# Kernel tuning notes

Hardware: AMD Instinct MI355X
Metric: run time of the kernel (lower is better)

Reference implementation:

```python
import jax
import jax.numpy as jnp
import numpy as np

N_WIRES = 4          # hardcoded by QLayer encoder (rx on wires 0..3)
H = N_WIRES          # hidden_dim must equal n_qubits for the gating elementwise math
T, B, D, TAGS = 512, 2048, 8, 16  # original unbinds dim 0, so dim0 = time, dim1 = batch


def apply_rx(state, theta, wire):
    """Apply RX(theta) on `wire`. state: (B,2,2,2,2) complex64, theta: (B,)."""
    st = jnp.moveaxis(state, 1 + wire, -1)
    a, b = st[..., 0], st[..., 1]
    th = theta[:, None, None, None] * 0.5
    c = jnp.cos(th)
    s = -1j * jnp.sin(th)
    st = jnp.stack([c * a + s * b, s * a + c * b], axis=-1)
    return jnp.moveaxis(st, -1, 1 + wire)


def apply_cnot(state, ctrl, tgt):
    st = jnp.moveaxis(state, (1 + ctrl, 1 + tgt), (-2, -1))  # (...,2,2)
    st = st.at[..., 1, :].set(st[..., 1, ::-1])
    return jnp.moveaxis(st, (-2, -1), (1 + ctrl, 1 + tgt))


def qlayer(angles, thetas):
    """QuantumQLSTM.QLayer: RX data encoding, trainable RX, CNOT ring, PauliZ expvals.
    angles: (B, 4) data angles; thetas: (4,) trainable RX angles -> (B, 4) expvals."""
    bsz = angles.shape[0]
    state = jnp.zeros((bsz, 16), jnp.complex64).at[:, 0].set(1.0)
    state = state.reshape(bsz, 2, 2, 2, 2)
    for w in range(N_WIRES):
        state = apply_rx(state, angles[:, w], w)
    for w in range(N_WIRES):
        state = apply_rx(state, jnp.broadcast_to(thetas[w], (bsz,)), w)
    for w in range(N_WIRES):  # cnot(w, w+1), last wraps to 0
        state = apply_cnot(state, w, (w + 1) % N_WIRES)
    probs = state.real ** 2 + state.imag ** 2  # (B,2,2,2,2)
    exps = []
    for w in range(N_WIRES):
        sign = jnp.array([1.0, -1.0], jnp.float32).reshape(
            [1] + [2 if i == w else 1 for i in range(N_WIRES)])
        exps.append(jnp.sum(probs * sign, axis=(1, 2, 3, 4)))
    return jnp.stack(exps, axis=-1)  # (B, 4)


def lstm_forward(x, w_gates, b_gates, rx_theta):
    # Faithful to torch: inputs.unbind(dim=0) -> scan over axis 0; batch = x.shape[1].
    bsz = x.shape[1]
    h0 = jnp.zeros((bsz, H), x.dtype)
    c0 = jnp.zeros((bsz, H), x.dtype)

    def step(carry, xt):
        hx, cx = carry
        comb = jnp.concatenate([xt, hx], axis=-1)                    # (B, D+H)
        pre = jnp.einsum('bd,gkd->gbk', comb, w_gates) + b_gates[:, None, :]  # (4,B,4)
        f = jax.nn.sigmoid(qlayer(pre[0], rx_theta[0]))
        i = jax.nn.sigmoid(qlayer(pre[1], rx_theta[1]))
        g = jnp.tanh(qlayer(pre[2], rx_theta[2]))
        o = jax.nn.sigmoid(qlayer(pre[3], rx_theta[3]))
        cx = f * cx + i * g
        hx = o * jnp.tanh(cx)
        return (hx, cx), hx

    _, outs = jax.lax.scan(jax.checkpoint(step), (h0, c0), x)
    return outs  # (T, B, H)


def setup_inputs() -> dict:
    key = jax.random.key(0)
    ks = jax.random.split(key, 6)
    x = jax.random.normal(ks[0], (T, B, D), jnp.float32)
    w_gates = jax.random.normal(ks[1], (4, N_WIRES, D + H), jnp.float32) * 0.3
    b_gates = jnp.zeros((4, N_WIRES), jnp.float32)
    rx_theta = jax.random.uniform(ks[2], (4, N_WIRES), jnp.float32, 0.0, 2.0 * np.pi)
    w_tag = jax.random.normal(ks[3], (TAGS, H), jnp.float32) * 0.3
    b_tag = jnp.zeros((TAGS,), jnp.float32)
    return {"x": x, "w_gates": w_gates, "b_gates": b_gates,
            "rx_theta": rx_theta, "w_tag": w_tag, "b_tag": b_tag}


def reference(x, w_gates, b_gates, rx_theta, w_tag, b_tag):
    # encode(): SamplerQNN has input_params=[], so it cannot transform features;
    # features pass through to the QLSTM (see notes).
    outs = lstm_forward(x, w_gates, b_gates, rx_theta)   # (T, B, H)
    logits = outs @ w_tag.T + b_tag                      # (T, B, TAGS)
    return jax.nn.log_softmax(logits, axis=-1)
```

## Files before the change

kernel.cpp:

```cpp
#include <hip/hip_runtime.h>

#define TT   512
#define BB   2048
#define NTAG 16
#define CH   8
#define NCH  (TT / CH)
#define BBN  (BB * NTAG)

typedef float v2f __attribute__((ext_vector_type(2)));

#define DPP_XOR1  0xB1
#define DPP_XOR2  0x4E
#define DPP_XOR3  0x1B
#define DPP_ROR4  0x124
#define DPP_ROR8  0x128
#define DPP_ROR12 0x12C

template<int CTRL>
__device__ __forceinline__ float dppf(float v) {
    int r = __builtin_amdgcn_update_dpp(0, __builtin_bit_cast(int, v),
                                        CTRL, 0xF, 0xF, true);
    return __builtin_bit_cast(float, r);
}

__global__ __launch_bounds__(256, 1) void qlstm_fused(
    const float* __restrict__ x,
    const float* __restrict__ w_gates,
    const float* __restrict__ b_gates,
    const float* __restrict__ rx_theta,
    const float* __restrict__ w_tag,
    const float* __restrict__ b_tag,
    float* __restrict__ out)
{
    __shared__ float4 lds4[2][2][CH][8];
    __shared__ float  hbuf[2][2][CH][64];

    const int tid = threadIdx.x;
    const int wv  = tid >> 6;
    const int l   = tid & 63;
    const int e   = l >> 4;
    const int g   = (l >> 2) & 3;
    const int k   = l & 3;

    const float IV  = 0.15915494309189535f;
    const float L2E = 1.44269504088896f;
    const float LN2 = 0.69314718056f;

    if (wv < 2) {
        const int b0 = blockIdx.x * 8 + wv * 4;

        const float* wrow = w_gates + (g * 4 + k) * 12;
        const v2f wp0 = { wrow[0] * IV, wrow[1] * IV };
        const v2f wp1 = { wrow[2] * IV, wrow[3] * IV };
        const v2f wp2 = { wrow[4] * IV, wrow[5] * IV };
        const v2f wp3 = { wrow[6] * IV, wrow[7] * IV };
        const float wh0 = wrow[8 + (k ^ 0)] * IV;
        const float wh1 = wrow[8 + (k ^ 1)] * IV;
        const float wh2 = wrow[8 + (k ^ 2)] * IV;
        const float wh3 = wrow[8 + (k ^ 3)] * IV;
        const v2f bp = { (b_gates[g * 4 + k] + rx_theta[g * 4 + k]) * IV, 0.0f };

        const bool gt = (g == 2);
        const float bA = gt ? 0.0f : 0.5f;
        const float d0 = gt ? 0.999904f  : 0.25f;
        const float d1 = gt ? -0.331065f : -0.0208333333f;
        const float d2 = gt ? 0.120472f  : 0.00208333333f;
        const float d3 = gt ? -0.027717f : -2.10813e-4f;

        const float u0 = 0.999160f,  u1 = -0.325289f, u2 = 0.112257f;
        const float u3 = -0.028766f, u4 = 0.0043665f, u5 = -0.00028186f;

        const bool k0 = (k == 0), k1 = (k == 1), k3 = (k == 3);
        const bool g0 = (g == 0), g2 = (g == 2), glo = (g < 2);

        const float* xlane = x + (size_t)(l >> 3) * (BB * 8)
                               + (size_t)b0 * 8 + (l & 7) * 4;
        const size_t CHOFF = (size_t)CH * BB * 8;
        float4* ldsw = (float4*)&lds4[wv][0][0][0];

        float4 reg = *(const float4*)(xlane);
        ldsw[l] = reg;
        reg = *(const float4*)(xlane + CHOFF);

        float4 xcA = lds4[wv][0][0][2 * e];
        float4 xcB = lds4[wv][0][0][2 * e + 1];

        float h = 0.f, c = 0.f, h1 = 0.f, h2 = 0.f, h3 = 0.f;

        for (int cc = 0; cc < NCH; ++cc) {
            const int cur = cc & 1;
            ldsw[(cur ^ 1) * 64 + l] = reg;
            const int cn = (cc + 2 < NCH) ? cc + 2 : NCH - 1;
            reg = *(const float4*)(xlane + (size_t)cn * CHOFF);

            #pragma unroll
            for (int i = 0; i < CH; ++i) {
                const int nb = (i == CH - 1) ? (cur ^ 1) : cur;
                const int ns = (i + 1) & (CH - 1);
                const float4 xnA = lds4[wv][nb][ns][2 * e];
                const float4 xnB = lds4[wv][nb][ns][2 * e + 1];

                const v2f a01 = { xcA.x, xcA.y }, a23 = { xcA.z, xcA.w };
                const v2f a45 = { xcB.x, xcB.y }, a67 = { xcB.z, xcB.w };
                v2f acc = __builtin_elementwise_fma(a01, wp0, bp);
                acc = __builtin_elementwise_fma(a23, wp1, acc);
                acc = __builtin_elementwise_fma(a45, wp2, acc);
                acc = __builtin_elementwise_fma(a67, wp3, acc);
                const float accx = acc.x + acc.y;

                float ang = fmaf(h,  wh0, accx);
                ang = fmaf(h1, wh1, ang);
                ang = fmaf(h2, wh2, ang);
                ang = fmaf(h3, wh3, ang);

                const float C = __builtin_amdgcn_cosf(ang);
                const float m1 = dppf<DPP_XOR1>(C);
                const float m2 = dppf<DPP_XOR2>(C);
                const float m3 = dppf<DPP_XOR3>(C);
                const float Bp = m2 * m3;
                const float pp = C * m1;
                const float X  = k0 ? m1 : (k3 ? pp : C);
                const float Y  = k1 ? m1 : Bp;
                const float q  = X * Y;

                const float y  = q * q;
                const float y2 = y * y;
                const float tA = fmaf(y, d1, d0);
                const float tB = fmaf(y, d3, d2);
                const float P  = fmaf(y2, tB, tA);
                const float act = fmaf(q, P, bA);

                const float rA = dppf<DPP_ROR12>(act);
                const float rB = dppf<DPP_ROR8>(act);
                const float rC = dppf<DPP_ROR4>(act);
                c = fmaf(act, c, rA * rB);

                const float cy  = c * c;
                const float cy2 = cy * cy;
                const float t1  = fmaf(cy, u1, u0);
                const float t2  = fmaf(cy, u3, u2);
                const float t3  = fmaf(cy, u5, u4);
                const float t4  = fmaf(cy2, t3, t2);
                const float Pc  = fmaf(cy2, t4, t1);
                const float voc = rC * c;
                const float h_raw = Pc * voc;

                hbuf[wv][cur][i][l] = h_raw;

                const float r4  = dppf<DPP_ROR4>(h_raw);
                const float r8  = dppf<DPP_ROR8>(h_raw);
                const float r12 = dppf<DPP_ROR12>(h_raw);
                h = glo ? (g0 ? h_raw : r4) : (g2 ? r8 : r12);

                h1 = dppf<DPP_XOR1>(h);
                h2 = dppf<DPP_XOR2>(h);
                h3 = dppf<DPP_XOR3>(h);

                xcA = xnA; xcB = xnB;
            }
            __syncthreads();
        }
    } else {
        const int pw = wv - 2;
        const int b0 = blockIdx.x * 8 + pw * 4;
        const int tag = g * 4 + k;

        const float wt0 = w_tag[tag * 4 + (k ^ 0)] * L2E;
        const float wt1 = w_tag[tag * 4 + (k ^ 1)] * L2E;
        const float wt2 = w_tag[tag * 4 + (k ^ 2)] * L2E;
        const float wt3 = w_tag[tag * 4 + (k ^ 3)] * L2E;
        const float bt  = b_tag[tag] * L2E;

        float* outp = out + (size_t)b0 * NTAG + l;
        const int hsl = e * 16 + k;

        for (int cc = 0; cc < NCH; ++cc) {
            __syncthreads();
            const int cur = cc & 1;

            #pragma unroll
            for (int i = 0; i < CH; ++i) {
                const float hv = hbuf[pw][cur][i][hsl];
                const float h1 = dppf<DPP_XOR1>(hv);
                const float h2 = dppf<DPP_XOR2>(hv);
                const float h3 = dppf<DPP_XOR3>(hv);

                const float lgq = fmaf(hv, wt0, fmaf(h1, wt1, fmaf(h2, wt2,
                                     fmaf(h3, wt3, bt))));
                const float ex = __builtin_amdgcn_exp2f(lgq);
                float s = ex + dppf<DPP_XOR1>(ex);
                s = s + dppf<DPP_XOR2>(s);
                s = s + dppf<DPP_ROR4>(s);
                s = s + dppf<DPP_ROR8>(s);
                const float l2s = __builtin_amdgcn_logf(s);

                *outp = (lgq - l2s) * LN2;
                outp += BBN;
            }
        }
    }
}

extern "C" void kernel_launch(void* const* d_in, const int* in_sizes, int n_in,
                              void* d_out, int out_size, void* d_ws, size_t ws_size,
                              hipStream_t stream) {
    const float* x        = (const float*)d_in[0];
    const float* w_gates  = (const float*)d_in[1];
    const float* b_gates  = (const float*)d_in[2];
    const float* rx_theta = (const float*)d_in[3];
    const float* w_tag    = (const float*)d_in[4];
    const float* b_tag    = (const float*)d_in[5];
    float* out = (float*)d_out;

    qlstm_fused<<<BB / 8, 256, 0, stream>>>(x, w_gates, b_gates, rx_theta,
                                            w_tag, b_tag, out);
}
```

Baseline: 150.1 us.

## Split recurrence into one wave with two interleaved chains plus producer/consumer waves

Restructures the block into one recurrence wave and two helper waves. The recurrence wave interleaves two independent batch groups (A/B) so their serial dependency chains can hide each other's latency. The helper waves precompute the input projection for the next chunk into LDS and emit log-softmax outputs for the previous chunk, which takes x loading and the input FMA off the critical path. In exchange it adds a one-chunk pipeline skew, more LDS traffic, and only three waves per block.

```diff
diff --git a/kernel.cpp b/kernel.cpp
--- a/kernel.cpp
+++ b/kernel.cpp
@@ -23,7 +23,7 @@
     return __builtin_bit_cast(float, r);
 }
 
-__global__ __launch_bounds__(256, 1) void qlstm_fused(
+__global__ __launch_bounds__(192, 1) void qlstm_fused(
     const float* __restrict__ x,
     const float* __restrict__ w_gates,
     const float* __restrict__ b_gates,
@@ -32,8 +32,9 @@
     const float* __restrict__ b_tag,
     float* __restrict__ out)
 {
-    __shared__ float4 lds4[2][2][CH][8];
-    __shared__ float  hbuf[2][2][CH][64];
+    __shared__ float  accL[2][2][CH][64];
+    __shared__ float  hrng[2][2][CH][64];
+    __shared__ float4 xstg[2][2][64];
 
     const int tid = threadIdx.x;
     const int wv  = tid >> 6;
@@ -46,153 +47,256 @@
     const float L2E = 1.44269504088896f;
     const float LN2 = 0.69314718056f;
 
-    if (wv < 2) {
-        const int b0 = blockIdx.x * 8 + wv * 4;
+    if (wv == 0) {
+        const float* wrow = w_gates + (g * 4 + k) * 12;
+        const float wh0 = wrow[8 + (k ^ 0)] * IV;
+        const float wh1 = wrow[8 + (k ^ 1)] * IV;
+        const float wh2 = wrow[8 + (k ^ 2)] * IV;
+        const float wh3 = wrow[8 + (k ^ 3)] * IV;
+
+        const bool gt = (g == 2);
+        const float ab = gt ? 0.0f : 0.5f;
+        const float d0 = gt ? 0.999904f  : 0.25f;
+        const float d1 = gt ? -0.331065f : -0.0208333333f;
+        const float d2 = gt ? 0.120472f  : 0.00208333333f;
+        const float d3 = gt ? -0.027717f : -2.10813e-4f;
+
+        const float u0 = 0.999160f,  u1 = -0.325289f, u2 = 0.112257f;
+        const float u3 = -0.028766f, u4 = 0.0043665f, u5 = -0.00028186f;
+
+        const bool k0 = (k == 0), k1 = (k == 1), k3 = (k == 3);
+        const bool g0 = (g == 0), g2 = (g == 2), glo = (g < 2);
+
+        float hA = 0.f, h1A = 0.f, h2A = 0.f, h3A = 0.f, cA = 0.f;
+        float hB = 0.f, h1B = 0.f, h2B = 0.f, h3B = 0.f, cB = 0.f;
+
+        __syncthreads();
+
+        for (int cc = 0; cc < NCH; ++cc) {
+            const int cur = cc & 1;
+            const float* apA = &accL[0][cur][0][l];
+            const float* apB = &accL[1][cur][0][l];
+            float* hpA = &hrng[0][cur][0][l];
+            float* hpB = &hrng[1][cur][0][l];
+
+            float aA = apA[0];
+            float aB = apB[0];
+
+            #pragma unroll
+            for (int i = 0; i < CH; ++i) {
+                float nA = aA, nB = aB;
+                if (i + 1 < CH) {
+                    nA = apA[(i + 1) * 64];
+                    nB = apB[(i + 1) * 64];
+                }
+
+                float angA = fmaf(hA, wh0, aA);
+                float angB = fmaf(hB, wh0, aB);
+                angA = fmaf(h1A, wh1, angA);
+                angB = fmaf(h1B, wh1, angB);
+                angA = fmaf(h2A, wh2, angA);
+                angB = fmaf(h2B, wh2, angB);
+                angA = fmaf(h3A, wh3, angA);
+                angB = fmaf(h3B, wh3, angB);
+
+                const float CA = __builtin_amdgcn_cosf(angA);
+                const float CB = __builtin_amdgcn_cosf(angB);
+
+                const float m1A = dppf<DPP_XOR1>(CA);
+                const float m1B = dppf<DPP_XOR1>(CB);
+                const float m2A = dppf<DPP_XOR2>(CA);
+                const float m2B = dppf<DPP_XOR2>(CB);
+                const float m3A = dppf<DPP_XOR3>(CA);
+                const float m3B = dppf<DPP_XOR3>(CB);
+                const float BpA = m2A * m3A;
+                const float BpB = m2B * m3B;
+                const float ppA = CA * m1A;
+                const float ppB = CB * m1B;
+                const float XA = k0 ? m1A : (k3 ? ppA : CA);
+                const float XB = k0 ? m1B : (k3 ? ppB : CB);
+                const float YA = k1 ? m1A : BpA;
+                const float YB = k1 ? m1B : BpB;
+                const float qA = XA * YA;
+                const float qB = XB * YB;
+
+                const float yA  = qA * qA;
+                const float yB  = qB * qB;
+                const float y2A = yA * yA;
+                const float y2B = yB * yB;
+                const float paA = fmaf(yA, d1, d0);
+                const float paB = fmaf(yB, d1, d0);
+                const float pbA = fmaf(yA, d3, d2);
+                const float pbB = fmaf(yB, d3, d2);
+                const float PA  = fmaf(y2A, pbA, paA);
+                const float PB  = fmaf(y2B, pbB, paB);
+                const float actA = fmaf(qA, PA, ab);
+                const float actB = fmaf(qB, PB, ab);
+
+                const float rAA = dppf<DPP_ROR12>(actA);
+                const float rAB = dppf<DPP_ROR12>(actB);
+                const float rBA = dppf<DPP_ROR8>(actA);
+                const float rBB = dppf<DPP_ROR8>(actB);
+                const float rCA = dppf<DPP_ROR4>(actA);
+                const float rCB = dppf<DPP_ROR4>(actB);
+                cA = fmaf(actA, cA, rAA * rBA);
+                cB = fmaf(actB, cB, rAB * rBB);
+
+                const float cyA  = cA * cA;
+                const float cyB  = cB * cB;
+                const float cy2A = cyA * cyA;
+                const float cy2B = cyB * cyB;
+                const float t1A = fmaf(cyA, u1, u0);
+                const float t1B = fmaf(cyB, u1, u0);
+                const float t2A = fmaf(cyA, u3, u2);
+                const float t2B = fmaf(cyB, u3, u2);
+                const float t3A = fmaf(cyA, u5, u4);
+                const float t3B = fmaf(cyB, u5, u4);
+                const float t4A = fmaf(cy2A, t3A, t2A);
+                const float t4B = fmaf(cy2B, t3B, t2B);
+                const float PcA = fmaf(cy2A, t4A, t1A);
+                const float PcB = fmaf(cy2B, t4B, t1B);
+                const float vocA = rCA * cA;
+                const float vocB = rCB * cB;
+                const float hrA = PcA * vocA;
+                const float hrB = PcB * vocB;
+
+                hpA[i * 64] = hrA;
+                hpB[i * 64] = hrB;
+
+                const float r4A  = dppf<DPP_ROR4>(hrA);
+                const float r4B  = dppf<DPP_ROR4>(hrB);
+                const float r8A  = dppf<DPP_ROR8>(hrA);
+                const float r8B  = dppf<DPP_ROR8>(hrB);
+                const float r12A = dppf<DPP_ROR12>(hrA);
+                const float r12B = dppf<DPP_ROR12>(hrB);
+                hA = glo ? (g0 ? hrA : r4A) : (g2 ? r8A : r12A);
+                hB = glo ? (g0 ? hrB : r4B) : (g2 ? r8B : r12B);
+
+                h1A = dppf<DPP_XOR1>(hA);
+                h1B = dppf<DPP_XOR1>(hB);
+                h2A = dppf<DPP_XOR2>(hA);
+                h2B = dppf<DPP_XOR2>(hB);
+                h3A = dppf<DPP_XOR3>(hA);
+                h3B = dppf<DPP_XOR3>(hB);
+
+                aA = nA; aB = nB;
+            }
+            __syncthreads();
+        }
+    } else {
+        const int s  = wv - 1;
+        const int b0 = blockIdx.x * 8 + s * 4;
 
         const float* wrow = w_gates + (g * 4 + k) * 12;
         const v2f wp0 = { wrow[0] * IV, wrow[1] * IV };
         const v2f wp1 = { wrow[2] * IV, wrow[3] * IV };
         const v2f wp2 = { wrow[4] * IV, wrow[5] * IV };
         const v2f wp3 = { wrow[6] * IV, wrow[7] * IV };
-        const float wh0 = wrow[8 + (k ^ 0)] * IV;
-        const float wh1 = wrow[8 + (k ^ 1)] * IV;
-        const float wh2 = wrow[8 + (k ^ 2)] * IV;
-        const float wh3 = wrow[8 + (k ^ 3)] * IV;
-        const v2f bp = { (b_gates[g * 4 + k] + rx_theta[g * 4 + k]) * IV, 0.0f };
-
-        const bool gt = (g == 2);
-        const float bA = gt ? 0.0f : 0.5f;
-        const float d0 = gt ? 0.999904f  : 0.25f;
-        const float d1 = gt ? -0.331065f : -0.0208333333f;
-        const float d2 = gt ? 0.120472f  : 0.00208333333f;
-        const float d3 = gt ? -0.027717f : -2.10813e-4f;
-
-        const float u0 = 0.999160f,  u1 = -0.325289f, u2 = 0.112257f;
-        const float u3 = -0.028766f, u4 = 0.0043665f, u5 = -0.00028186f;
-
-        const bool k0 = (k == 0), k1 = (k == 1), k3 = (k == 3);
-        const bool g0 = (g == 0), g2 = (g == 2), glo = (g < 2);
-
-        const float* xlane = x + (size_t)(l >> 3) * (BB * 8)
-                               + (size_t)b0 * 8 + (l & 7) * 4;
-        const size_t CHOFF = (size_t)CH * BB * 8;
-        float4* ldsw = (float4*)&lds4[wv][0][0][0];
-
-        float4 reg = *(const float4*)(xlane);
-        ldsw[l] = reg;
-        reg = *(const float4*)(xlane + CHOFF);
-
-        float4 xcA = lds4[wv][0][0][2 * e];
-        float4 xcB = lds4[wv][0][0][2 * e + 1];
-
-        float h = 0.f, c = 0.f, h1 = 0.f, h2 = 0.f, h3 = 0.f;
-
-        for (int cc = 0; cc < NCH; ++cc) {
-            const int cur = cc & 1;
-            ldsw[(cur ^ 1) * 64 + l] = reg;
-            const int cn = (cc + 2 < NCH) ? cc + 2 : NCH - 1;
-            reg = *(const float4*)(xlane + (size_t)cn * CHOFF);
-
-            #pragma unroll
-            for (int i = 0; i < CH; ++i) {
-                const int nb = (i == CH - 1) ? (cur ^ 1) : cur;
-                const int ns = (i + 1) & (CH - 1);
-                const float4 xnA = lds4[wv][nb][ns][2 * e];
-                const float4 xnB = lds4[wv][nb][ns][2 * e + 1];
-
-                const v2f a01 = { xcA.x, xcA.y }, a23 = { xcA.z, xcA.w };
-                const v2f a45 = { xcB.x, xcB.y }, a67 = { xcB.z, xcB.w };
-                v2f acc = __builtin_elementwise_fma(a01, wp0, bp);
-                acc = __builtin_elementwise_fma(a23, wp1, acc);
-                acc = __builtin_elementwise_fma(a45, wp2, acc);
-                acc = __builtin_elementwise_fma(a67, wp3, acc);
-                const float accx = acc.x + acc.y;
-
-                float ang = fmaf(h,  wh0, accx);
-                ang = fmaf(h1, wh1, ang);
-                ang = fmaf(h2, wh2, ang);
-                ang = fmaf(h3, wh3, ang);
-
-                const float C = __builtin_amdgcn_cosf(ang);
-                const float m1 = dppf<DPP_XOR1>(C);
-                const float m2 = dppf<DPP_XOR2>(C);
-                const float m3 = dppf<DPP_XOR3>(C);
-                const float Bp = m2 * m3;
-                const float pp = C * m1;
-                const float X  = k0 ? m1 : (k3 ? pp : C);
-                const float Y  = k1 ? m1 : Bp;
-                const float q  = X * Y;
-
-                const float y  = q * q;
-                const float y2 = y * y;
-                const float tA = fmaf(y, d1, d0);
-                const float tB = fmaf(y, d3, d2);
-                const float P  = fmaf(y2, tB, tA);
-                const float act = fmaf(q, P, bA);
-
-                const float rA = dppf<DPP_ROR12>(act);
-                const float rB = dppf<DPP_ROR8>(act);
-                const float rC = dppf<DPP_ROR4>(act);
-                c = fmaf(act, c, rA * rB);
-
-                const float cy  = c * c;
-                const float cy2 = cy * cy;
-                const float t1  = fmaf(cy, u1, u0);
-                const float t2  = fmaf(cy, u3, u2);
-                const float t3  = fmaf(cy, u5, u4);
-                const float t4  = fmaf(cy2, t3, t2);
-                const float Pc  = fmaf(cy2, t4, t1);
-                const float voc = rC * c;
-                const float h_raw = Pc * voc;
-
-                hbuf[wv][cur][i][l] = h_raw;
-
-                const float r4  = dppf<DPP_ROR4>(h_raw);
-                const float r8  = dppf<DPP_ROR8>(h_raw);
-                const float r12 = dppf<DPP_ROR12>(h_raw);
-                h = glo ? (g0 ? h_raw : r4) : (g2 ? r8 : r12);
-
-                h1 = dppf<DPP_XOR1>(h);
-                h2 = dppf<DPP_XOR2>(h);
-                h3 = dppf<DPP_XOR3>(h);
-
-                xcA = xnA; xcB = xnB;
-            }
-            __syncthreads();
-        }
-    } else {
-        const int pw = wv - 2;
-        const int b0 = blockIdx.x * 8 + pw * 4;
+        const v2f bp  = { (b_gates[g * 4 + k] + rx_theta[g * 4 + k]) * IV, 0.0f };
+
         const int tag = g * 4 + k;
-
         const float wt0 = w_tag[tag * 4 + (k ^ 0)] * L2E;
         const float wt1 = w_tag[tag * 4 + (k ^ 1)] * L2E;
         const float wt2 = w_tag[tag * 4 + (k ^ 2)] * L2E;
         const float wt3 = w_tag[tag * 4 + (k ^ 3)] * L2E;
         const float bt  = b_tag[tag] * L2E;
 
+        const int hsl = e * 16 + k;
         float* outp = out + (size_t)b0 * NTAG + l;
-        const int hsl = e * 16 + k;
-
-        for (int cc = 0; cc < NCH; ++cc) {
-            __syncthreads();
-            const int cur = cc & 1;
-
+
+        const float* xlane = x + (size_t)(l >> 3) * (BB * 8)
+                               + (size_t)b0 * 8 + (l & 7) * 4;
+        const size_t CHOFF = (size_t)CH * BB * 8;
+
+        float4 reg = *(const float4*)(xlane);
+        xstg[s][0][l] = reg;
+        reg = *(const float4*)(xlane + CHOFF);
+        xstg[s][1][l] = reg;
+        {
+            float* ap = &accL[s][0][0][l];
             #pragma unroll
             for (int i = 0; i < CH; ++i) {
-                const float hv = hbuf[pw][cur][i][hsl];
-                const float h1 = dppf<DPP_XOR1>(hv);
-                const float h2 = dppf<DPP_XOR2>(hv);
-                const float h3 = dppf<DPP_XOR3>(hv);
-
-                const float lgq = fmaf(hv, wt0, fmaf(h1, wt1, fmaf(h2, wt2,
-                                     fmaf(h3, wt3, bt))));
+                const float4 xA = xstg[s][0][i * 8 + 2 * e];
+                const float4 xB = xstg[s][0][i * 8 + 2 * e + 1];
+                const v2f a01 = { xA.x, xA.y }, a23 = { xA.z, xA.w };
+                const v2f a45 = { xB.x, xB.y }, a67 = { xB.z, xB.w };
+                v2f acc = __builtin_elementwise_fma(a01, wp0, bp);
+                acc = __builtin_elementwise_fma(a23, wp1, acc);
+                acc = __builtin_elementwise_fma(a45, wp2, acc);
+                acc = __builtin_elementwise_fma(a67, wp3, acc);
+                ap[i * 64] = acc.x + acc.y;
+            }
+        }
+        reg = *(const float4*)(xlane + 2 * CHOFF);
+        __syncthreads();
+
+        for (int cc = 0; cc < NCH; ++cc) {
+            const int cur = cc & 1;
+
+            if (cc + 2 < NCH) {
+                xstg[s][cur][l] = reg;
+                const int cn = (cc + 3 < NCH) ? cc + 3 : NCH - 1;
+                reg = *(const float4*)(xlane + (size_t)cn * CHOFF);
+            }
+
+            if (cc + 1 < NCH) {
+                float* ap = &accL[s][cur ^ 1][0][l];
+                #pragma unroll
+                for (int i = 0; i < CH; ++i) {
+                    const float4 xA = xstg[s][cur ^ 1][i * 8 + 2 * e];
+                    const float4 xB = xstg[s][cur ^ 1][i * 8 + 2 * e + 1];
+                    const v2f a01 = { xA.x, xA.y }, a23 = { xA.z, xA.w };
+                    const v2f a45 = { xB.x, xB.y }, a67 = { xB.z, xB.w };
+                    v2f acc = __builtin_elementwise_fma(a01, wp0, bp);
+                    acc = __builtin_elementwise_fma(a23, wp1, acc);
+                    acc = __builtin_elementwise_fma(a45, wp2, acc);
+                    acc = __builtin_elementwise_fma(a67, wp3, acc);
+                    ap[i * 64] = acc.x + acc.y;
+                }
+            }
+
+            if (cc > 0) {
+                const float* hp = &hrng[s][cur ^ 1][0][hsl];
+                #pragma unroll
+                for (int i = 0; i < CH; ++i) {
+                    const float hv = hp[i * 64];
+                    const float q1 = dppf<DPP_XOR1>(hv);
+                    const float q2 = dppf<DPP_XOR2>(hv);
+                    const float q3 = dppf<DPP_XOR3>(hv);
+
+                    const float lgq = fmaf(hv, wt0, fmaf(q1, wt1, fmaf(q2, wt2,
+                                         fmaf(q3, wt3, bt))));
+                    const float ex = __builtin_amdgcn_exp2f(lgq);
+                    float sm = ex + dppf<DPP_XOR1>(ex);
+                    sm = sm + dppf<DPP_XOR2>(sm);
+                    sm = sm + dppf<DPP_ROR4>(sm);
+                    sm = sm + dppf<DPP_ROR8>(sm);
+                    const float l2s = __builtin_amdgcn_logf(sm);
+
+                    *outp = (lgq - l2s) * LN2;
+                    outp += BBN;
+                }
+            }
+            __syncthreads();
+        }
+
+        {
+            const float* hp = &hrng[s][1][0][hsl];
+            #pragma unroll
+            for (int i = 0; i < CH; ++i) {
+                const float hv = hp[i * 64];
+                const float q1 = dppf<DPP_XOR1>(hv);
+                const float q2 = dppf<DPP_XOR2>(hv);
+                const float q3 = dppf<DPP_XOR3>(hv);
+
+                const float lgq = fmaf(hv, wt0, fmaf(q1, wt1, fmaf(q2, wt2,
+                                     fmaf(q3, wt3, bt))));
                 const float ex = __builtin_amdgcn_exp2f(lgq);
-                float s = ex + dppf<DPP_XOR1>(ex);
-                s = s + dppf<DPP_XOR2>(s);
-                s = s + dppf<DPP_ROR4>(s);
-                s = s + dppf<DPP_ROR8>(s);
-                const float l2s = __builtin_amdgcn_logf(s);
+                float sm = ex + dppf<DPP_XOR1>(ex);
+                sm = sm + dppf<DPP_XOR2>(sm);
+                sm = sm + dppf<DPP_ROR4>(sm);
+                sm = sm + dppf<DPP_ROR8>(sm);
+                const float l2s = __builtin_amdgcn_logf(sm);
 
                 *outp = (lgq - l2s) * LN2;
                 outp += BBN;
@@ -212,6 +316,6 @@
     const float* b_tag    = (const float*)d_in[5];
     float* out = (float*)d_out;
 
-    qlstm_fused<<<BB / 8, 256, 0, stream>>>(x, w_gates, b_gates, rx_theta,
+    qlstm_fused<<<BB / 8, 192, 0, stream>>>(x, w_gates, b_gates, rx_theta,
                                             w_tag, b_tag, out);
 }
```

New measurement: 170.0 us. 1.13x slower.
